# Kernel tuning notes

Hardware: AMD Instinct MI355X
Metric: run time of the kernel (lower is better)

Reference implementation:

```python
import jax, jax.numpy as jnp
import numpy as np

B, S, E, H, W, G = 1, 2048, 1024, 16, 512, 16
HD = E // H

def setup_inputs() -> dict:
    key = jax.random.key(0)
    ks = jax.random.split(key, 12)
    s = 1.0 / np.sqrt(E)
    inp = {
        'query': jax.random.normal(ks[0], (B, S, E), jnp.float32),
        'key':   jax.random.normal(ks[1], (B, S, E), jnp.float32),
        'value': jax.random.normal(ks[2], (B, S, E), jnp.float32),
        'is_global': jnp.broadcast_to(jnp.arange(S) < G, (B, S)),
        'Wq': jax.random.uniform(ks[3], (E, E), jnp.float32, -s, s),
        'bq': jax.random.uniform(ks[4], (E,),   jnp.float32, -s, s),
        'Wk': jax.random.uniform(ks[5], (E, E), jnp.float32, -s, s),
        'bk': jax.random.uniform(ks[6], (E,),   jnp.float32, -s, s),
        'Wv': jax.random.uniform(ks[7], (E, E), jnp.float32, -s, s),
        'bv': jax.random.uniform(ks[8], (E,),   jnp.float32, -s, s),
        'Wo': jax.random.uniform(ks[9], (E, E), jnp.float32, -s, s),
        'bo': jax.random.uniform(ks[10], (E,),  jnp.float32, -s, s),
    }
    return inp

def reference(query, key, value, is_global, Wq, bq, Wk, bk, Wv, bv, Wo, bo):
    # Linear projections (torch Linear: x @ W.T + b), reshape to [B,H,S,HD]
    def proj(x, Wt, b):
        return (x @ Wt.T + b).reshape(B, S, H, HD).transpose(0, 2, 1, 3)
    q = proj(query, Wq, bq)
    k = proj(key,   Wk, bk)
    v = proj(value, Wv, bv)

    scores = jnp.einsum('bhqd,bhkd->bhqk', q, k) / np.sqrt(HD)  # [B,H,S,S]

    idx = jnp.arange(S)
    window_mask = jnp.abs(idx[None, :] - idx[:, None]) <= W      # [S,S]
    combined = (window_mask[None, None]
                | is_global[:, None, None, :]    # global keys
                | is_global[:, None, :, None])   # global queries
    scores = jnp.where(combined, scores, -jnp.inf)

    attn = jax.nn.softmax(scores, axis=-1)  # dropout is identity in eval
    out = jnp.einsum('bhqk,bhkd->bhqd', attn, v)
    out = out.transpose(0, 2, 1, 3).reshape(B, S, E)
    return out @ Wo.T + bo
```

## Files before the change

### kernel.cpp

```cpp
#include <hip/hip_runtime.h>
#include <hip/hip_bf16.h>
#include <stdint.h>

#define S_LEN 2048
#define E_DIM 1024
#define N_HEAD 16
#define HD 64
#define WIN 512

typedef __attribute__((ext_vector_type(4))) float f32x4;
typedef __attribute__((ext_vector_type(8))) short bf16x8;
typedef __attribute__((ext_vector_type(8))) unsigned short u16x8;

__device__ __forceinline__ unsigned f2bf2(float lo, float hi) {
  __hip_bfloat162 h = __float22bfloat162_rn(make_float2(lo, hi));
  return *reinterpret_cast<unsigned*>(&h);
}
__device__ __forceinline__ unsigned short f2bf(float f) {
  __hip_bfloat16 h = __float2bfloat16(f);
  return *reinterpret_cast<unsigned short*>(&h);
}
__device__ __forceinline__ float bf2f(unsigned short u) {
  union { unsigned u; float f; } v; v.u = (unsigned)u << 16; return v.f;
}

__device__ __forceinline__ void gl2lds16(const void* g, void* l) {
  __builtin_amdgcn_global_load_lds((const __attribute__((address_space(1))) void*)g,
                                   (__attribute__((address_space(3))) void*)l, 16, 0, 0);
}

__global__ __launch_bounds__(256) void convert_kernel(
    const float* __restrict__ q, const float* __restrict__ k, const float* __restrict__ v,
    const float* __restrict__ wq, const float* __restrict__ wk,
    const float* __restrict__ wv, const float* __restrict__ wo,
    unsigned short* __restrict__ dst, const int* __restrict__ gm,
    unsigned char* __restrict__ kmask, unsigned char* __restrict__ bflag) {
  const size_t SE = (size_t)S_LEN * E_DIM, EE = (size_t)E_DIM * E_DIM;
  if (blockIdx.x == 0) {
    __shared__ int badw;
    int tid = threadIdx.x;
    if (tid == 0) badw = 0;
    __syncthreads();
    for (int i = tid; i < S_LEN / 4; i += 256) {
      int vv = gm[i];
      if (vv != 0 && vv != 1) atomicOr(&badw, 1);
    }
    __syncthreads();
    const int bytes = badw;
    const unsigned char* gb = (const unsigned char*)gm;
    for (int i = tid; i < S_LEN; i += 256)
      kmask[i] = bytes ? (unsigned char)(gb[i] != 0) : (unsigned char)(gm[i] != 0);
    if (tid < S_LEN / 64) {
      unsigned char any = 0;
      for (int j = 0; j < 64; ++j) {
        int i = tid * 64 + j;
        any |= bytes ? (unsigned char)(gb[i] != 0) : (unsigned char)(gm[i] != 0);
      }
      bflag[tid] = any;
    }
  }
  size_t i = ((size_t)blockIdx.x * 256 + threadIdx.x) * 8;
  const float* src;
  size_t off;
  if (i < SE) { src = q; off = i; }
  else if (i < 2 * SE) { src = k; off = i - SE; }
  else if (i < 3 * SE) { src = v; off = i - 2 * SE; }
  else if (i < 3 * SE + EE) { src = wq; off = i - 3 * SE; }
  else if (i < 3 * SE + 2 * EE) { src = wk; off = i - 3 * SE - EE; }
  else if (i < 3 * SE + 3 * EE) { src = wv; off = i - 3 * SE - 2 * EE; }
  else { src = wo; off = i - 3 * SE - 3 * EE; }
  f32x4 x0 = *(const f32x4*)(src + off);
  f32x4 x1 = *(const f32x4*)(src + off + 4);
  union { u16x8 v; unsigned u[4]; } o;
  o.u[0] = f2bf2(x0[0], x0[1]); o.u[1] = f2bf2(x0[2], x0[3]);
  o.u[2] = f2bf2(x1[0], x1[1]); o.u[3] = f2bf2(x1[2], x1[3]);
  *(u16x8*)(dst + i) = o.v;
}

template <int BM, int BN, int OUTMODE>
__device__ __forceinline__ void gemm_body(const unsigned short* __restrict__ A,
                                          const unsigned short* __restrict__ B,
                                          const float* __restrict__ bias,
                                          void* __restrict__ Out_) {
  __shared__ unsigned short As[BM][64];
  __shared__ unsigned short Bs[BN][64];
  constexpr int MI = (BM == 128) ? 4 : 2;
  const int tid = threadIdx.x;
  const int wid = tid >> 6, lane = tid & 63;
  const int a = lane & 15, g = lane >> 4;
  const int m0 = blockIdx.y * BM, n0 = blockIdx.x * BN;
  const int wr = (wid >> 1) * (BM / 2);
  const int wc = (wid & 1) * 64;
  const int l8 = lane >> 3, l7 = (lane & 7) * 8;
  f32x4 acc[MI][4] = {};

  for (int k0 = 0; k0 < E_DIM; k0 += 64) {
    __syncthreads();
#pragma unroll
    for (int c = 0; c < BM / 32; ++c) {
      const int r0 = (wid * (BM / 32) + c) * 8;
      gl2lds16(A + (size_t)(m0 + r0 + l8) * E_DIM + k0 + l7, &As[r0][0]);
    }
#pragma unroll
    for (int c = 0; c < BN / 32; ++c) {
      const int r0 = (wid * (BN / 32) + c) * 8;
      gl2lds16(B + (size_t)(n0 + r0 + l8) * E_DIM + k0 + l7, &Bs[r0][0]);
    }
    __syncthreads();
#pragma unroll
    for (int s = 0; s < 2; ++s) {
      bf16x8 af[MI], bfv[4];
#pragma unroll
      for (int i = 0; i < MI; ++i) af[i] = *(const bf16x8*)&As[wr + i * 16 + a][s * 32 + g * 8];
#pragma unroll
      for (int j = 0; j < 4; ++j) bfv[j] = *(const bf16x8*)&Bs[wc + j * 16 + a][s * 32 + g * 8];
#pragma unroll
      for (int i = 0; i < MI; ++i)
#pragma unroll
        for (int j = 0; j < 4; ++j)
          acc[i][j] = __builtin_amdgcn_mfma_f32_16x16x32_bf16(af[i], bfv[j], acc[i][j], 0, 0, 0);
    }
  }
#pragma unroll
  for (int i = 0; i < MI; ++i)
#pragma unroll
    for (int j = 0; j < 4; ++j) {
      const int row0 = m0 + wr + i * 16 + g * 4;
      const int col = n0 + wc + j * 16 + a;
      if (OUTMODE == 2) {
        unsigned short* O = (unsigned short*)Out_;
        unsigned lo = f2bf2(acc[i][j][0] + bias[col], acc[i][j][1] + bias[col]);
        unsigned hi = f2bf2(acc[i][j][2] + bias[col], acc[i][j][3] + bias[col]);
        uint2 pk; pk.x = lo; pk.y = hi;
        *(uint2*)&O[(size_t)col * S_LEN + row0] = pk;
      } else {
#pragma unroll
        for (int r = 0; r < 4; ++r) {
          float v = acc[i][j][r] + bias[col];
          if (OUTMODE == 0) {
            unsigned short* O = (unsigned short*)Out_;
            O[((size_t)(col >> 6) * S_LEN + row0 + r) * HD + (col & 63)] = f2bf(v);
          } else {
            float* O = (float*)Out_;
            O[(size_t)(row0 + r) * E_DIM + col] = v;
          }
        }
      }
    }
}

__global__ __launch_bounds__(256) void gemm_qkv_kernel(
    const unsigned short* __restrict__ wsbf, const float* __restrict__ bq,
    const float* __restrict__ bk, const float* __restrict__ bv,
    unsigned short* __restrict__ Qo, unsigned short* __restrict__ Ko,
    unsigned short* __restrict__ Vo) {
  const size_t SE = (size_t)S_LEN * E_DIM, EE = (size_t)E_DIM * E_DIM;
  const int z = blockIdx.z;
  const unsigned short* A = wsbf + (size_t)z * SE;
  const unsigned short* W = wsbf + 3 * SE + (size_t)z * EE;
  const float* b = z == 0 ? bq : (z == 1 ? bk : bv);
  if (z == 2)
    gemm_body<128, 128, 2>(A, W, b, Vo);
  else
    gemm_body<128, 128, 0>(A, W, b, z == 0 ? Qo : Ko);
}

__global__ __launch_bounds__(256) void gemm_out_kernel(
    const unsigned short* __restrict__ Oi, const unsigned short* __restrict__ Wo,
    const float* __restrict__ bo, float* __restrict__ out) {
  gemm_body<64, 128, 1>(Oi, Wo, bo, out);
}

__global__ __launch_bounds__(256) void attn_win_kernel(
    const unsigned short* __restrict__ Q, const unsigned short* __restrict__ K,
    const unsigned short* __restrict__ Vt_g, const unsigned char* __restrict__ kmask,
    const unsigned char* __restrict__ bflag, unsigned short* __restrict__ O) {
  __shared__ unsigned short Kt[128][72];
  __shared__ unsigned short Vt[64][136];
  __shared__ float Plf[4][16][132];
  __shared__ unsigned char kmAll[S_LEN];

  const int tid = threadIdx.x;
  const int wid = tid >> 6, lane = tid & 63;
  const int a = lane & 15, g = lane >> 4;

  const int fid = blockIdx.x + (blockIdx.y << 5);
  const int logical = ((fid & 7) << 6) + (fid >> 3);
  const int h = logical >> 5;
  const int q0 = (logical & 31) << 6;
  const int qw = q0 + wid * 16;

  ((uint2*)kmAll)[tid] = ((const uint2*)kmask)[tid];

  const size_t qbase = ((size_t)h * S_LEN + (qw + a)) * HD;
  const bf16x8 qf0 = *(const bf16x8*)(Q + qbase + g * 8);
  const bf16x8 qf1 = *(const bf16x8*)(Q + qbase + 32 + g * 8);

  __syncthreads();
  int qg[4];
#pragma unroll
  for (int r = 0; r < 4; ++r) qg[r] = kmAll[qw + g * 4 + r];

  unsigned amask = 0;
  {
    int lo = (q0 - WIN) >> 7; if (lo < 0) lo = 0;
    int hi = (q0 + 63 + WIN) >> 7; if (hi > 15) hi = 15;
#pragma unroll
    for (int t2 = 0; t2 < 16; ++t2) {
      bool act = (t2 >= lo && t2 <= hi) || bflag[2 * t2] || bflag[2 * t2 + 1];
      amask |= (unsigned)act << t2;
    }
  }

  float m[4], l[4];
  f32x4 acc[4];
#pragma unroll
  for (int r = 0; r < 4; ++r) { m[r] = -1e30f; l[r] = 0.f; }
#pragma unroll
  for (int d = 0; d < 4; ++d) acc[d] = f32x4{0.f, 0.f, 0.f, 0.f};

  const unsigned short* Kh = K + (size_t)h * S_LEN * HD;
  const unsigned short* Vh = Vt_g + (size_t)h * HD * S_LEN;
  const float c = 0.18033688011112042f;

  u16x8 kreg[4], vreg[4];
  auto issue = [&](int k0) {
    const u16x8* pk = (const u16x8*)(Kh + (size_t)(k0 + (tid >> 1)) * HD + (tid & 1) * 32);
    kreg[0] = pk[0]; kreg[1] = pk[1]; kreg[2] = pk[2]; kreg[3] = pk[3];
    const u16x8* pv = (const u16x8*)(Vh + (size_t)(tid >> 2) * S_LEN + k0 + (tid & 3) * 32);
    vreg[0] = pv[0]; vreg[1] = pv[1]; vreg[2] = pv[2]; vreg[3] = pv[3];
  };

  int kb = amask ? __builtin_ctz(amask) : 16;
  if (kb < 16) issue(kb * 128);
  while (kb < 16) {
    const unsigned rem = amask >> (kb + 1);
    const int nxt = rem ? kb + 1 + __builtin_ctz(rem) : 16;
    const int k0 = kb * 128;

    __syncthreads();
    {
      u16x8* dk = (u16x8*)&Kt[tid >> 1][(tid & 1) * 32];
      dk[0] = kreg[0]; dk[1] = kreg[1]; dk[2] = kreg[2]; dk[3] = kreg[3];
      u16x8* dv = (u16x8*)&Vt[tid >> 2][(tid & 3) * 32];
      dv[0] = vreg[0]; dv[1] = vreg[1]; dv[2] = vreg[2]; dv[3] = vreg[3];
    }
    __syncthreads();
    if (nxt < 16) issue(nxt * 128);

    f32x4 s4[8];
    __builtin_amdgcn_s_setprio(1);
#pragma unroll
    for (int t = 0; t < 8; ++t) {
      bf16x8 kf0 = *(const bf16x8*)&Kt[t * 16 + a][g * 8];
      bf16x8 kf1 = *(const bf16x8*)&Kt[t * 16 + a][32 + g * 8];
      f32x4 z = {0.f, 0.f, 0.f, 0.f};
      z = __builtin_amdgcn_mfma_f32_16x16x32_bf16(qf0, kf0, z, 0, 0, 0);
      z = __builtin_amdgcn_mfma_f32_16x16x32_bf16(qf1, kf1, z, 0, 0, 0);
      s4[t] = z;
    }
    __builtin_amdgcn_s_setprio(0);

    float tv[8][4];
    const bool interior = (k0 >= q0 - 449) && (k0 <= q0 + 385);
    if (interior) {
#pragma unroll
      for (int t = 0; t < 8; ++t)
#pragma unroll
        for (int r = 0; r < 4; ++r) tv[t][r] = s4[t][r] * c;
    } else {
#pragma unroll
      for (int t = 0; t < 8; ++t) {
        const int kc = k0 + t * 16 + a;
        const int kglob = kmAll[kc];
#pragma unroll
        for (int r = 0; r < 4; ++r) {
          const int qr = qw + g * 4 + r;
          bool inc = qg[r] || kglob || ((unsigned)(qr - kc + WIN) <= (unsigned)(2 * WIN));
          tv[t][r] = inc ? s4[t][r] * c : -3.0e38f;
        }
      }
    }

#pragma unroll
    for (int r = 0; r < 4; ++r) {
      float tm = fmaxf(fmaxf(tv[0][r], tv[1][r]), fmaxf(tv[2][r], tv[3][r]));
      tm = fmaxf(tm, fmaxf(fmaxf(tv[4][r], tv[5][r]), fmaxf(tv[6][r], tv[7][r])));
#pragma unroll
      for (int off = 1; off < 16; off <<= 1) tm = fmaxf(tm, __shfl_xor(tm, off, 16));
      const float mn = fmaxf(m[r], tm);
      const float rs = __builtin_amdgcn_exp2f(m[r] - mn);
      m[r] = mn;
      float ps = 0.f;
#pragma unroll
      for (int t = 0; t < 8; ++t) {
        float p = __builtin_amdgcn_exp2f(tv[t][r] - mn);
        tv[t][r] = p; ps += p;
      }
#pragma unroll
      for (int off = 1; off < 16; off <<= 1) ps += __shfl_xor(ps, off, 16);
      l[r] = l[r] * rs + ps;
#pragma unroll
      for (int d = 0; d < 4; ++d) acc[d][r] *= rs;
    }

#pragma unroll
    for (int t = 0; t < 8; ++t)
#pragma unroll
      for (int r = 0; r < 4; ++r)
        Plf[wid][g * 4 + r][t * 16 + a] = tv[t][r];
    bf16x8 pa[4];
#pragma unroll
    for (int ks = 0; ks < 4; ++ks) {
      const float* pp = &Plf[wid][a][ks * 32 + g * 8];
      f32x4 x0 = *(const f32x4*)pp, x1 = *(const f32x4*)(pp + 4);
      union { bf16x8 v; unsigned u[4]; } pu;
      pu.u[0] = f2bf2(x0[0], x0[1]); pu.u[1] = f2bf2(x0[2], x0[3]);
      pu.u[2] = f2bf2(x1[0], x1[1]); pu.u[3] = f2bf2(x1[2], x1[3]);
      pa[ks] = pu.v;
    }

    __builtin_amdgcn_s_setprio(1);
#pragma unroll
    for (int d = 0; d < 4; ++d)
#pragma unroll
      for (int ks = 0; ks < 4; ++ks) {
        bf16x8 vf = *(const bf16x8*)&Vt[d * 16 + a][ks * 32 + g * 8];
        acc[d] = __builtin_amdgcn_mfma_f32_16x16x32_bf16(pa[ks], vf, acc[d], 0, 0, 0);
      }
    __builtin_amdgcn_s_setprio(0);
    kb = nxt;
  }

#pragma unroll
  for (int d = 0; d < 4; ++d)
#pragma unroll
    for (int r = 0; r < 4; ++r) {
      const int qr = qw + g * 4 + r;
      float v = acc[d][r] / l[r];
      O[(size_t)qr * E_DIM + h * HD + d * 16 + a] = f2bf(v);
    }
}

__global__ __launch_bounds__(256) void attn_glb_kernel(
    const unsigned short* __restrict__ Q, const unsigned short* __restrict__ K,
    const unsigned short* __restrict__ Vt_g, unsigned short* __restrict__ PA,
    float2* __restrict__ ML) {
  __shared__ float Plf[4][16][68];

  const int tid = threadIdx.x;
  const int wid = tid >> 6, lane = tid & 63;
  const int a = lane & 15, g = lane >> 4;
  const int h = blockIdx.y;
  const int split = blockIdx.x * 4 + wid;
  const int k0 = split * 64;

  const size_t qb = ((size_t)h * S_LEN + a) * HD;
  const bf16x8 qf0 = *(const bf16x8*)(Q + qb + g * 8);
  const bf16x8 qf1 = *(const bf16x8*)(Q + qb + 32 + g * 8);

  const unsigned short* Kh = K + (size_t)h * S_LEN * HD;
  const unsigned short* Vh = Vt_g + (size_t)h * HD * S_LEN;
  const float c = 0.18033688011112042f;

  f32x4 s4[4];
#pragma unroll
  for (int t = 0; t < 4; ++t) {
    const unsigned short* kp = Kh + (size_t)(k0 + t * 16 + a) * HD;
    bf16x8 kf0 = *(const bf16x8*)(kp + g * 8);
    bf16x8 kf1 = *(const bf16x8*)(kp + 32 + g * 8);
    f32x4 z = {0.f, 0.f, 0.f, 0.f};
    z = __builtin_amdgcn_mfma_f32_16x16x32_bf16(qf0, kf0, z, 0, 0, 0);
    z = __builtin_amdgcn_mfma_f32_16x16x32_bf16(qf1, kf1, z, 0, 0, 0);
    s4[t] = z;
  }

  float m[4], l[4];
  float tv[4][4];
#pragma unroll
  for (int t = 0; t < 4; ++t)
#pragma unroll
    for (int r = 0; r < 4; ++r) tv[t][r] = s4[t][r] * c;
#pragma unroll
  for (int r = 0; r < 4; ++r) {
    float tm = fmaxf(fmaxf(tv[0][r], tv[1][r]), fmaxf(tv[2][r], tv[3][r]));
#pragma unroll
    for (int off = 1; off < 16; off <<= 1) tm = fmaxf(tm, __shfl_xor(tm, off, 16));
    float ps = 0.f;
#pragma unroll
    for (int t = 0; t < 4; ++t) {
      float p = __builtin_amdgcn_exp2f(tv[t][r] - tm);
      tv[t][r] = p; ps += p;
    }
#pragma unroll
    for (int off = 1; off < 16; off <<= 1) ps += __shfl_xor(ps, off, 16);
    m[r] = tm; l[r] = ps;
  }

#pragma unroll
  for (int t = 0; t < 4; ++t)
#pragma unroll
    for (int r = 0; r < 4; ++r)
      Plf[wid][g * 4 + r][t * 16 + a] = tv[t][r];
  bf16x8 pa[2];
#pragma unroll
  for (int ks = 0; ks < 2; ++ks) {
    const float* pp = &Plf[wid][a][ks * 32 + g * 8];
    f32x4 x0 = *(const f32x4*)pp, x1 = *(const f32x4*)(pp + 4);
    union { bf16x8 v; unsigned u[4]; } pu;
    pu.u[0] = f2bf2(x0[0], x0[1]); pu.u[1] = f2bf2(x0[2], x0[3]);
    pu.u[2] = f2bf2(x1[0], x1[1]); pu.u[3] = f2bf2(x1[2], x1[3]);
    pa[ks] = pu.v;
  }

  f32x4 acc[4] = {};
#pragma unroll
  for (int d = 0; d < 4; ++d)
#pragma unroll
    for (int ks = 0; ks < 2; ++ks) {
      bf16x8 vf = *(const bf16x8*)(Vh + (size_t)(d * 16 + a) * S_LEN + k0 + ks * 32 + g * 8);
      acc[d] = __builtin_amdgcn_mfma_f32_16x16x32_bf16(pa[ks], vf, acc[d], 0, 0, 0);
    }

  unsigned short* pacc = PA + (((size_t)h * 32 + split) * 16) * 64;
#pragma unroll
  for (int d = 0; d < 4; ++d)
#pragma unroll
    for (int r = 0; r < 4; ++r)
      pacc[(g * 4 + r) * 64 + d * 16 + a] = f2bf(acc[d][r]);
  if (a == 0) {
    float2* pml = ML + ((size_t)h * 32 + split) * 16;
#pragma unroll
    for (int r = 0; r < 4; ++r) pml[g * 4 + r] = make_float2(m[r], l[r]);
  }
}

__global__ __launch_bounds__(256) void combine_glb_kernel(
    const unsigned short* __restrict__ PA, const float2* __restrict__ ML,
    unsigned short* __restrict__ O) {
  const int h = blockIdx.x, tid = threadIdx.x;
  const int row = tid >> 4, d0 = (tid & 15) * 4;
  float M = -1e30f;
#pragma unroll 8
  for (int s = 0; s < 32; ++s) M = fmaxf(M, ML[((size_t)h * 32 + s) * 16 + row].x);
  float L = 0.f, o0 = 0.f, o1 = 0.f, o2 = 0.f, o3 = 0.f;
  for (int s = 0; s < 32; ++s) {
    float2 ml = ML[((size_t)h * 32 + s) * 16 + row];
    float w = __builtin_amdgcn_exp2f(ml.x - M);
    L += w * ml.y;
    const unsigned short* p = PA + (((size_t)h * 32 + s) * 16 + row) * 64 + d0;
    o0 += w * bf2f(p[0]); o1 += w * bf2f(p[1]);
    o2 += w * bf2f(p[2]); o3 += w * bf2f(p[3]);
  }
  const float inv = 1.0f / L;
  uint2 pk;
  pk.x = f2bf2(o0 * inv, o1 * inv);
  pk.y = f2bf2(o2 * inv, o3 * inv);
  *(uint2*)&O[(size_t)row * E_DIM + h * HD + d0] = pk;
}

extern "C" void kernel_launch(void* const* d_in, const int* in_sizes, int n_in,
                              void* d_out, int out_size, void* d_ws, size_t ws_size,
                              hipStream_t stream) {
  const float* q  = (const float*)d_in[0];
  const float* k  = (const float*)d_in[1];
  const float* v  = (const float*)d_in[2];
  const int* isg  = (const int*)d_in[3];
  const float* Wq = (const float*)d_in[4];
  const float* bq = (const float*)d_in[5];
  const float* Wk = (const float*)d_in[6];
  const float* bk = (const float*)d_in[7];
  const float* Wv = (const float*)d_in[8];
  const float* bv = (const float*)d_in[9];
  const float* Wo = (const float*)d_in[10];
  const float* bo = (const float*)d_in[11];

  const size_t SE = (size_t)S_LEN * E_DIM, EE = (size_t)E_DIM * E_DIM;
  unsigned short* wsbf = (unsigned short*)d_ws;
  unsigned short* Qb = wsbf + 3 * SE + 4 * EE;
  unsigned short* Kb = Qb + SE;
  unsigned short* Vb = Kb + SE;
  unsigned short* Ob = wsbf;
  unsigned char* kmask = (unsigned char*)(Vb + SE);
  unsigned char* bflag = kmask + S_LEN;
  unsigned short* PA = wsbf + SE;
  float2* ML = (float2*)(PA + (size_t)16 * 32 * 16 * 64);

  const int total_conv_blocks = (int)((3 * SE + 4 * EE) / (256 * 8));
  convert_kernel<<<total_conv_blocks, 256, 0, stream>>>(q, k, v, Wq, Wk, Wv, Wo, wsbf,
                                                        isg, kmask, bflag);
  gemm_qkv_kernel<<<dim3(E_DIM / 128, S_LEN / 128, 3), 256, 0, stream>>>(
      wsbf, bq, bk, bv, Qb, Kb, Vb);
  attn_win_kernel<<<dim3(S_LEN / 64, N_HEAD), 256, 0, stream>>>(Qb, Kb, Vb, kmask, bflag, Ob);
  attn_glb_kernel<<<dim3(8, N_HEAD), 256, 0, stream>>>(Qb, Kb, Vb, PA, ML);
  combine_glb_kernel<<<N_HEAD, 256, 0, stream>>>(PA, ML, Ob);
  gemm_out_kernel<<<dim3(E_DIM / 128, S_LEN / 64), 256, 0, stream>>>(
      Ob, wsbf + 3 * SE + 3 * EE, bo, (float*)d_out);
}
```

Measured before the change: 125.9 us.

## Merge global-attention blocks into window kernel and shrink GEMM tiles for occupancy

```diff
diff --git a/kernel.cpp b/kernel.cpp
--- a/kernel.cpp
+++ b/kernel.cpp
@@ -77,28 +77,28 @@
   *(u16x8*)(dst + i) = o.v;
 }
 
-template <int BM, int BN, int OUTMODE>
+template <int BN, int OUTMODE>
 __device__ __forceinline__ void gemm_body(const unsigned short* __restrict__ A,
                                           const unsigned short* __restrict__ B,
                                           const float* __restrict__ bias,
                                           void* __restrict__ Out_) {
-  __shared__ unsigned short As[BM][64];
+  __shared__ unsigned short As[64][64];
   __shared__ unsigned short Bs[BN][64];
-  constexpr int MI = (BM == 128) ? 4 : 2;
+  constexpr int MI = (BN == 128) ? 2 : 1;
   const int tid = threadIdx.x;
   const int wid = tid >> 6, lane = tid & 63;
   const int a = lane & 15, g = lane >> 4;
-  const int m0 = blockIdx.y * BM, n0 = blockIdx.x * BN;
-  const int wr = (wid >> 1) * (BM / 2);
-  const int wc = (wid & 1) * 64;
+  const int m0 = blockIdx.y * 64, n0 = blockIdx.x * BN;
+  const int wr = (BN == 128) ? (wid >> 1) * 32 : wid * 16;
+  const int wc = (BN == 128) ? (wid & 1) * 64 : 0;
   const int l8 = lane >> 3, l7 = (lane & 7) * 8;
   f32x4 acc[MI][4] = {};
 
   for (int k0 = 0; k0 < E_DIM; k0 += 64) {
     __syncthreads();
 #pragma unroll
-    for (int c = 0; c < BM / 32; ++c) {
-      const int r0 = (wid * (BM / 32) + c) * 8;
+    for (int c = 0; c < 2; ++c) {
+      const int r0 = (wid * 2 + c) * 8;
       gl2lds16(A + (size_t)(m0 + r0 + l8) * E_DIM + k0 + l7, &As[r0][0]);
     }
 #pragma unroll
@@ -160,21 +160,22 @@
   const unsigned short* W = wsbf + 3 * SE + (size_t)z * EE;
   const float* b = z == 0 ? bq : (z == 1 ? bk : bv);
   if (z == 2)
-    gemm_body<128, 128, 2>(A, W, b, Vo);
+    gemm_body<128, 2>(A, W, b, Vo);
   else
-    gemm_body<128, 128, 0>(A, W, b, z == 0 ? Qo : Ko);
+    gemm_body<128, 0>(A, W, b, z == 0 ? Qo : Ko);
 }
 
 __global__ __launch_bounds__(256) void gemm_out_kernel(
     const unsigned short* __restrict__ Oi, const unsigned short* __restrict__ Wo,
     const float* __restrict__ bo, float* __restrict__ out) {
-  gemm_body<64, 128, 1>(Oi, Wo, bo, out);
-}
-
-__global__ __launch_bounds__(256) void attn_win_kernel(
+  gemm_body<64, 1>(Oi, Wo, bo, out);
+}
+
+__global__ __launch_bounds__(256) void attn_kernel(
     const unsigned short* __restrict__ Q, const unsigned short* __restrict__ K,
     const unsigned short* __restrict__ Vt_g, const unsigned char* __restrict__ kmask,
-    const unsigned char* __restrict__ bflag, unsigned short* __restrict__ O) {
+    const unsigned char* __restrict__ bflag, unsigned short* __restrict__ O,
+    unsigned short* __restrict__ PA, float2* __restrict__ ML) {
   __shared__ unsigned short Kt[128][72];
   __shared__ unsigned short Vt[64][136];
   __shared__ float Plf[4][16][132];
@@ -183,6 +184,86 @@
   const int tid = threadIdx.x;
   const int wid = tid >> 6, lane = tid & 63;
   const int a = lane & 15, g = lane >> 4;
+
+  if (blockIdx.x >= 32) {
+    const int h = blockIdx.y;
+    const int split = (blockIdx.x - 32) * 4 + wid;
+    const int k0 = split * 64;
+    const unsigned short* Kh = K + (size_t)h * S_LEN * HD;
+    const unsigned short* Vh = Vt_g + (size_t)h * HD * S_LEN;
+    const float c = 0.18033688011112042f;
+
+    const size_t qb = ((size_t)h * S_LEN + a) * HD;
+    const bf16x8 qf0 = *(const bf16x8*)(Q + qb + g * 8);
+    const bf16x8 qf1 = *(const bf16x8*)(Q + qb + 32 + g * 8);
+
+    f32x4 s4[4];
+#pragma unroll
+    for (int t = 0; t < 4; ++t) {
+      const unsigned short* kp = Kh + (size_t)(k0 + t * 16 + a) * HD;
+      bf16x8 kf0 = *(const bf16x8*)(kp + g * 8);
+      bf16x8 kf1 = *(const bf16x8*)(kp + 32 + g * 8);
+      f32x4 z = {0.f, 0.f, 0.f, 0.f};
+      z = __builtin_amdgcn_mfma_f32_16x16x32_bf16(qf0, kf0, z, 0, 0, 0);
+      z = __builtin_amdgcn_mfma_f32_16x16x32_bf16(qf1, kf1, z, 0, 0, 0);
+      s4[t] = z;
+    }
+    float m[4], l[4], tv[4][4];
+#pragma unroll
+    for (int t = 0; t < 4; ++t)
+#pragma unroll
+      for (int r = 0; r < 4; ++r) tv[t][r] = s4[t][r] * c;
+#pragma unroll
+    for (int r = 0; r < 4; ++r) {
+      float tm = fmaxf(fmaxf(tv[0][r], tv[1][r]), fmaxf(tv[2][r], tv[3][r]));
+#pragma unroll
+      for (int off = 1; off < 16; off <<= 1) tm = fmaxf(tm, __shfl_xor(tm, off, 16));
+      float ps = 0.f;
+#pragma unroll
+      for (int t = 0; t < 4; ++t) {
+        float p = __builtin_amdgcn_exp2f(tv[t][r] - tm);
+        tv[t][r] = p; ps += p;
+      }
+#pragma unroll
+      for (int off = 1; off < 16; off <<= 1) ps += __shfl_xor(ps, off, 16);
+      m[r] = tm; l[r] = ps;
+    }
+#pragma unroll
+    for (int t = 0; t < 4; ++t)
+#pragma unroll
+      for (int r = 0; r < 4; ++r)
+        Plf[wid][g * 4 + r][t * 16 + a] = tv[t][r];
+    bf16x8 pa[2];
+#pragma unroll
+    for (int ks = 0; ks < 2; ++ks) {
+      const float* pp = &Plf[wid][a][ks * 32 + g * 8];
+      f32x4 x0 = *(const f32x4*)pp, x1 = *(const f32x4*)(pp + 4);
+      union { bf16x8 v; unsigned u[4]; } pu;
+      pu.u[0] = f2bf2(x0[0], x0[1]); pu.u[1] = f2bf2(x0[2], x0[3]);
+      pu.u[2] = f2bf2(x1[0], x1[1]); pu.u[3] = f2bf2(x1[2], x1[3]);
+      pa[ks] = pu.v;
+    }
+    f32x4 acc[4] = {};
+#pragma unroll
+    for (int d = 0; d < 4; ++d)
+#pragma unroll
+      for (int ks = 0; ks < 2; ++ks) {
+        bf16x8 vf = *(const bf16x8*)(Vh + (size_t)(d * 16 + a) * S_LEN + k0 + ks * 32 + g * 8);
+        acc[d] = __builtin_amdgcn_mfma_f32_16x16x32_bf16(pa[ks], vf, acc[d], 0, 0, 0);
+      }
+    unsigned short* pacc = PA + (((size_t)h * 32 + split) * 16) * 64;
+#pragma unroll
+    for (int d = 0; d < 4; ++d)
+#pragma unroll
+      for (int r = 0; r < 4; ++r)
+        pacc[(g * 4 + r) * 64 + d * 16 + a] = f2bf(acc[d][r]);
+    if (a == 0) {
+      float2* pml = ML + ((size_t)h * 32 + split) * 16;
+#pragma unroll
+      for (int r = 0; r < 4; ++r) pml[g * 4 + r] = make_float2(m[r], l[r]);
+    }
+    return;
+  }
 
   const int fid = blockIdx.x + (blockIdx.y << 5);
   const int logical = ((fid & 7) << 6) + (fid >> 3);
@@ -340,99 +421,6 @@
       float v = acc[d][r] / l[r];
       O[(size_t)qr * E_DIM + h * HD + d * 16 + a] = f2bf(v);
     }
-}
-
-__global__ __launch_bounds__(256) void attn_glb_kernel(
-    const unsigned short* __restrict__ Q, const unsigned short* __restrict__ K,
-    const unsigned short* __restrict__ Vt_g, unsigned short* __restrict__ PA,
-    float2* __restrict__ ML) {
-  __shared__ float Plf[4][16][68];
-
-  const int tid = threadIdx.x;
-  const int wid = tid >> 6, lane = tid & 63;
-  const int a = lane & 15, g = lane >> 4;
-  const int h = blockIdx.y;
-  const int split = blockIdx.x * 4 + wid;
-  const int k0 = split * 64;
-
-  const size_t qb = ((size_t)h * S_LEN + a) * HD;
-  const bf16x8 qf0 = *(const bf16x8*)(Q + qb + g * 8);
-  const bf16x8 qf1 = *(const bf16x8*)(Q + qb + 32 + g * 8);
-
-  const unsigned short* Kh = K + (size_t)h * S_LEN * HD;
-  const unsigned short* Vh = Vt_g + (size_t)h * HD * S_LEN;
-  const float c = 0.18033688011112042f;
-
-  f32x4 s4[4];
-#pragma unroll
-  for (int t = 0; t < 4; ++t) {
-    const unsigned short* kp = Kh + (size_t)(k0 + t * 16 + a) * HD;
-    bf16x8 kf0 = *(const bf16x8*)(kp + g * 8);
-    bf16x8 kf1 = *(const bf16x8*)(kp + 32 + g * 8);
-    f32x4 z = {0.f, 0.f, 0.f, 0.f};
-    z = __builtin_amdgcn_mfma_f32_16x16x32_bf16(qf0, kf0, z, 0, 0, 0);
-    z = __builtin_amdgcn_mfma_f32_16x16x32_bf16(qf1, kf1, z, 0, 0, 0);
-    s4[t] = z;
-  }
-
-  float m[4], l[4];
-  float tv[4][4];
-#pragma unroll
-  for (int t = 0; t < 4; ++t)
-#pragma unroll
-    for (int r = 0; r < 4; ++r) tv[t][r] = s4[t][r] * c;
-#pragma unroll
-  for (int r = 0; r < 4; ++r) {
-    float tm = fmaxf(fmaxf(tv[0][r], tv[1][r]), fmaxf(tv[2][r], tv[3][r]));
-#pragma unroll
-    for (int off = 1; off < 16; off <<= 1) tm = fmaxf(tm, __shfl_xor(tm, off, 16));
-    float ps = 0.f;
-#pragma unroll
-    for (int t = 0; t < 4; ++t) {
-      float p = __builtin_amdgcn_exp2f(tv[t][r] - tm);
-      tv[t][r] = p; ps += p;
-    }
-#pragma unroll
-    for (int off = 1; off < 16; off <<= 1) ps += __shfl_xor(ps, off, 16);
-    m[r] = tm; l[r] = ps;
-  }
-
-#pragma unroll
-  for (int t = 0; t < 4; ++t)
-#pragma unroll
-    for (int r = 0; r < 4; ++r)
-      Plf[wid][g * 4 + r][t * 16 + a] = tv[t][r];
-  bf16x8 pa[2];
-#pragma unroll
-  for (int ks = 0; ks < 2; ++ks) {
-    const float* pp = &Plf[wid][a][ks * 32 + g * 8];
-    f32x4 x0 = *(const f32x4*)pp, x1 = *(const f32x4*)(pp + 4);
-    union { bf16x8 v; unsigned u[4]; } pu;
-    pu.u[0] = f2bf2(x0[0], x0[1]); pu.u[1] = f2bf2(x0[2], x0[3]);
-    pu.u[2] = f2bf2(x1[0], x1[1]); pu.u[3] = f2bf2(x1[2], x1[3]);
-    pa[ks] = pu.v;
-  }
-
-  f32x4 acc[4] = {};
-#pragma unroll
-  for (int d = 0; d < 4; ++d)
-#pragma unroll
-    for (int ks = 0; ks < 2; ++ks) {
-      bf16x8 vf = *(const bf16x8*)(Vh + (size_t)(d * 16 + a) * S_LEN + k0 + ks * 32 + g * 8);
-      acc[d] = __builtin_amdgcn_mfma_f32_16x16x32_bf16(pa[ks], vf, acc[d], 0, 0, 0);
-    }
-
-  unsigned short* pacc = PA + (((size_t)h * 32 + split) * 16) * 64;
-#pragma unroll
-  for (int d = 0; d < 4; ++d)
-#pragma unroll
-    for (int r = 0; r < 4; ++r)
-      pacc[(g * 4 + r) * 64 + d * 16 + a] = f2bf(acc[d][r]);
-  if (a == 0) {
-    float2* pml = ML + ((size_t)h * 32 + split) * 16;
-#pragma unroll
-    for (int r = 0; r < 4; ++r) pml[g * 4 + r] = make_float2(m[r], l[r]);
-  }
 }
 
 __global__ __launch_bounds__(256) void combine_glb_kernel(
@@ -489,11 +477,10 @@
   const int total_conv_blocks = (int)((3 * SE + 4 * EE) / (256 * 8));
   convert_kernel<<<total_conv_blocks, 256, 0, stream>>>(q, k, v, Wq, Wk, Wv, Wo, wsbf,
                                                         isg, kmask, bflag);
-  gemm_qkv_kernel<<<dim3(E_DIM / 128, S_LEN / 128, 3), 256, 0, stream>>>(
+  gemm_qkv_kernel<<<dim3(E_DIM / 128, S_LEN / 64, 3), 256, 0, stream>>>(
       wsbf, bq, bk, bv, Qb, Kb, Vb);
-  attn_win_kernel<<<dim3(S_LEN / 64, N_HEAD), 256, 0, stream>>>(Qb, Kb, Vb, kmask, bflag, Ob);
-  attn_glb_kernel<<<dim3(8, N_HEAD), 256, 0, stream>>>(Qb, Kb, Vb, PA, ML);
+  attn_kernel<<<dim3(40, N_HEAD), 256, 0, stream>>>(Qb, Kb, Vb, kmask, bflag, Ob, PA, ML);
   combine_glb_kernel<<<N_HEAD, 256, 0, stream>>>(PA, ML, Ob);
-  gemm_out_kernel<<<dim3(E_DIM / 128, S_LEN / 64), 256, 0, stream>>>(
+  gemm_out_kernel<<<dim3(E_DIM / 64, S_LEN / 64), 256, 0, stream>>>(
       Ob, wsbf + 3 * SE + 3 * EE, bo, (float*)d_out);
 }
```

Result: faster. 117.6 us (-6.6%).
